# Kernel optimization log

Hardware: AMD Instinct MI355X
Metric: run time of the kernel (lower is better)

Reference implementation:

```python
import jax, jax.numpy as jnp
import numpy as np
import math

SR = 16000
FFT = 1024
WIN = 640
HOP = 320
NMEL = 40
NCEP = 13
B = 1024
NS = 16000
F_MIN = 0.0
F_MAX = 8000.0
LIFT_L = 22.0
DELTA_N = 2


def _linear_to_mel_weight_matrix(num_mel, num_spec_bins, sr, fmin, fmax):
    # Exact replica of tf.signal.linear_to_mel_weight_matrix (HTK mel scale).
    def hz_to_mel(f):
        return 1127.0 * np.log1p(np.asarray(f, np.float64) / 700.0)
    nyquist = sr / 2.0
    lin_freqs = np.linspace(0.0, nyquist, num_spec_bins)
    spec_mel = hz_to_mel(lin_freqs[1:])[:, None]          # drop DC bin
    edges = np.linspace(hz_to_mel(fmin), hz_to_mel(fmax), num_mel + 2)
    lower, center, upper = edges[:-2], edges[1:-1], edges[2:]
    lower_slope = (spec_mel - lower) / (center - lower)
    upper_slope = (upper - spec_mel) / (upper - center)
    w = np.maximum(0.0, np.minimum(lower_slope, upper_slope))
    w = np.pad(w, ((1, 0), (0, 0)))                       # re-add zero DC row
    return w.astype(np.float32)


def setup_inputs() -> dict:
    key = jax.random.key(0)
    waveforms = jax.random.normal(key, (B, NS), dtype=jnp.float32)
    mel_fb = jnp.asarray(_linear_to_mel_weight_matrix(NMEL, FFT // 2 + 1, SR, F_MIN, F_MAX))
    return {"waveforms": waveforms, "mel_fb": mel_fb}


def _delta(feat, N):
    # feat: (B, T, C). Replicate-pad N frames at both ends, then weighted
    # sliding-window sum with weights k in [-N..N] (vectorized, no map_fn).
    T = feat.shape[1]
    denom = 2.0 * sum(float(k * k) for k in range(1, N + 1))
    padded = jnp.concatenate(
        [jnp.repeat(feat[:, :1, :], N, axis=1), feat,
         jnp.repeat(feat[:, -1:, :], N, axis=1)], axis=1)
    acc = jnp.zeros_like(feat)
    for k in range(-N, N + 1):
        if k != 0:
            acc = acc + float(k) * padded[:, N + k:N + k + T, :]
    return acc / denom


def reference(waveforms, mel_fb):
    # --- STFT (tf.signal.stft: periodic Hann, no pad_end, zero-pad to FFT) ---
    n = jnp.arange(WIN, dtype=jnp.float32)
    window = 0.5 - 0.5 * jnp.cos(2.0 * math.pi * n / WIN)
    num_frames = 1 + (NS - WIN) // HOP                    # 49
    idx = jnp.arange(num_frames)[:, None] * HOP + jnp.arange(WIN)[None, :]
    frames = waveforms[:, idx] * window
    frames = jnp.pad(frames, ((0, 0), (0, 0), (0, FFT - WIN)))
    spec = jnp.abs(jnp.fft.rfft(frames, n=FFT, axis=-1))  # (B, T, 513)

    # --- mel + log ---
    log_mel = jnp.log(spec @ mel_fb + 1e-6)               # (B, T, NMEL)

    # --- MFCC: DCT-II scaled by rsqrt(2*NMEL), keep first NCEP coeffs ---
    m = jnp.arange(NMEL, dtype=jnp.float32)[:, None]
    k = jnp.arange(NCEP, dtype=jnp.float32)[None, :]
    dct_mat = 2.0 * jnp.cos(math.pi * (2.0 * m + 1.0) * k / (2.0 * NMEL))
    mfccs = (log_mel @ dct_mat) * (1.0 / math.sqrt(2.0 * NMEL))

    # --- liftering ---
    c = jnp.arange(NCEP, dtype=jnp.float32)
    lift = 1.0 + (LIFT_L / 2.0) * jnp.sin(math.pi * c / LIFT_L)
    mfccs = mfccs * lift

    # --- deltas and delta-deltas ---
    d1 = _delta(mfccs, DELTA_N)
    d2 = _delta(d1, DELTA_N)
    out = jnp.concatenate([mfccs, d1, d2], axis=2)        # (B, T, 3*NCEP)
    return out[..., None]                                 # (B, T, 39, 1)
```

## Files before the change

### kernel.cpp

```cpp
#include <hip/hip_runtime.h>
#include <math.h>

#define NMEL   40
#define NCEP   13
#define BATCH  1024
#define NSAMP  16000
#define NFRAME 49
#define PI_F   3.14159265358979323846f

#define WS_WIN  0
#define WS_R    640
#define WS_DT   1664
#define WS_BT   2184
#define WS_TOT  15240

typedef _Float16 half8 __attribute__((ext_vector_type(8)));
typedef __fp16   fp16x2 __attribute__((ext_vector_type(2)));
typedef float f32x4 __attribute__((ext_vector_type(4)));

#define WAVE_FENCE() { __builtin_amdgcn_wave_barrier(); asm volatile("" ::: "memory"); }

#define BFLY(i0, i1, wr, wi) {                        \
    float tr = zr[i0] - zr[i1], ti = zi[i0] - zi[i1]; \
    zr[i0] += zr[i1]; zi[i0] += zi[i1];               \
    zr[i1] = tr*(wr) - ti*(wi);                       \
    zi[i1] = tr*(wi) + ti*(wr); }

__device__ __forceinline__ unsigned pk_f16(float a, float b) {
    fp16x2 h = __builtin_amdgcn_cvt_pkrtz(a, b);
    union { fp16x2 h; unsigned u; } cvt; cvt.h = h;
    return cvt.u;
}

__global__ __launch_bounds__(256) void mfcc_prep(
    const float* __restrict__ mel_fb, float* __restrict__ ws)
{
    const int idx = blockIdx.x * 256 + threadIdx.x;

    _Float16* bt = (_Float16*)(ws + WS_BT);
    for (int i = idx; i < 48 * 544; i += 64 * 256) {
        int n = i / 544, k = i - n * 544;
        float v = (n < NMEL && k < 513) ? mel_fb[k * NMEL + n] : 0.0f;
        bt[i] = (_Float16)v;
    }

    if (idx < 640 + 512 + 520) {
        int i = idx;
        if (i < 640) {
            ws[WS_WIN + i] = 0.5f - 0.5f * cosf(2.0f * PI_F * (float)i / 640.0f);
        } else if (i < 1152) {
            int k = i - 640;
            float s, c;
            sincosf(-2.0f * PI_F * (float)k / 1024.0f, &s, &c);
            ((float2*)(ws + WS_R))[k] = make_float2(c, s);
        } else {
            int j = i - 1152;
            int m = j / 13, c0 = j - m * 13;
            float d    = 2.0f * cosf(PI_F * (2.0f * m + 1.0f) * (float)c0 / 80.0f);
            float lift = 1.0f + 11.0f * sinf(PI_F * (float)c0 / 22.0f);
            ws[WS_DT + j] = d * 0.11180339887498949f * lift;
        }
    }
}

__global__ __launch_bounds__(256) void mfcc_stage1(
    const float* __restrict__ wave, const float* __restrict__ ws,
    float* __restrict__ out)
{
    __shared__ __align__(16) char smem[4 * 640 * 8 + 16 * 40 * 2];
    char* smemc = smem;
    _Float16* lm = (_Float16*)(smem + 4 * 640 * 8);

    const int tid = threadIdx.x;
    const int wv  = tid >> 6;
    const int L   = tid & 63;
    const int s   = L & 7;
    const int a   = L >> 3;

    float2* Z = (float2*)smem + wv * 640;
    const float2* R   = (const float2*)(ws + WS_R);
    const float2* win = (const float2*)(ws + WS_WIN);

    float2 twA[4], twB[2], twC, twD[4], twE[2], twF, twS[8], winv[5];
    #pragma unroll
    for (int j = 0; j < 4; ++j) twA[j] = R[2 * (L + 64 * j)];
    #pragma unroll
    for (int j = 0; j < 2; ++j) twB[j] = R[4 * (L + 64 * j)];
    twC = R[8 * L];
    #pragma unroll
    for (int j = 0; j < 4; ++j) twD[j] = R[128 * j + 16 * s];
    #pragma unroll
    for (int j = 0; j < 2; ++j) twE[j] = R[256 * j + 32 * s];
    twF = R[64 * s];
    #pragma unroll
    for (int j = 0; j < 8; ++j) twS[j] = R[8 * L + j];
    #pragma unroll
    for (int j = 0; j < 5; ++j) winv[j] = win[L + 64 * j];

    uint4 mgp[4];
    float m512v[4] = {0.0f, 0.0f, 0.0f, 0.0f};

    #pragma unroll
    for (int fi = 0; fi < 4; ++fi) {
        const int frame = blockIdx.x * 16 + wv * 4 + fi;
        const int b = frame / NFRAME;
        const int f = frame - b * NFRAME;
        const float2* xin = (const float2*)(wave + (size_t)b * NSAMP + (size_t)f * 320);

        float zr[8], zi[8];
        #pragma unroll
        for (int j = 0; j < 8; ++j) { zr[j] = 0.0f; zi[j] = 0.0f; }
        #pragma unroll
        for (int j = 0; j < 5; ++j) {
            float2 x = xin[L + 64 * j];
            zr[j] = x.x * winv[j].x;
            zi[j] = x.y * winv[j].y;
        }

        #pragma unroll
        for (int j = 0; j < 4; ++j) BFLY(j, j + 4, twA[j].x, twA[j].y);
        #pragma unroll
        for (int g = 0; g < 8; g += 4) {
            #pragma unroll
            for (int j = 0; j < 2; ++j) BFLY(g + j, g + j + 2, twB[j].x, twB[j].y);
        }
        #pragma unroll
        for (int i0 = 0; i0 < 8; i0 += 2) BFLY(i0, i0 + 1, twC.x, twC.y);

        WAVE_FENCE();
        #pragma unroll
        for (int j = 0; j < 8; ++j)
            Z[80 * j + 10 * s + a] = make_float2(zr[j], zi[j]);
        WAVE_FENCE();
        {
            float4 q0 = *(float4*)&Z[10 * L + 0];
            float4 q1 = *(float4*)&Z[10 * L + 2];
            float4 q2 = *(float4*)&Z[10 * L + 4];
            float4 q3 = *(float4*)&Z[10 * L + 6];
            zr[0] = q0.x; zi[0] = q0.y; zr[1] = q0.z; zi[1] = q0.w;
            zr[2] = q1.x; zi[2] = q1.y; zr[3] = q1.z; zi[3] = q1.w;
            zr[4] = q2.x; zi[4] = q2.y; zr[5] = q2.z; zi[5] = q2.w;
            zr[6] = q3.x; zi[6] = q3.y; zr[7] = q3.z; zi[7] = q3.w;
        }

        #pragma unroll
        for (int j = 0; j < 4; ++j) BFLY(j, j + 4, twD[j].x, twD[j].y);
        #pragma unroll
        for (int g = 0; g < 8; g += 4) {
            #pragma unroll
            for (int j = 0; j < 2; ++j) BFLY(g + j, g + j + 2, twE[j].x, twE[j].y);
        }
        #pragma unroll
        for (int i0 = 0; i0 < 8; i0 += 2) BFLY(i0, i0 + 1, twF.x, twF.y);

        WAVE_FENCE();
        #pragma unroll
        for (int j = 0; j < 8; ++j)
            Z[80 * a + 10 * j + s] = make_float2(zr[j], zi[j]);
        WAVE_FENCE();
        {
            float4 q0 = *(float4*)&Z[10 * L + 0];
            float4 q1 = *(float4*)&Z[10 * L + 2];
            float4 q2 = *(float4*)&Z[10 * L + 4];
            float4 q3 = *(float4*)&Z[10 * L + 6];
            zr[0] = q0.x; zi[0] = q0.y; zr[1] = q0.z; zi[1] = q0.w;
            zr[2] = q1.x; zi[2] = q1.y; zr[3] = q1.z; zi[3] = q1.w;
            zr[4] = q2.x; zi[4] = q2.y; zr[5] = q2.z; zi[5] = q2.w;
            zr[6] = q3.x; zi[6] = q3.y; zr[7] = q3.z; zi[7] = q3.w;
        }

        {
            const float C = 0.70710678118654752f;
            const float w8r[4] = { 1.0f,  C, 0.0f, -C };
            const float w8i[4] = { 0.0f, -C, -1.0f, -C };
            #pragma unroll
            for (int j = 0; j < 4; ++j) BFLY(j, j + 4, w8r[j], w8i[j]);
            #pragma unroll
            for (int g = 0; g < 8; g += 4) {
                BFLY(g + 0, g + 2, 1.0f, 0.0f);
                BFLY(g + 1, g + 3, 0.0f, -1.0f);
            }
            #pragma unroll
            for (int i0 = 0; i0 < 8; i0 += 2) BFLY(i0, i0 + 1, 1.0f, 0.0f);
        }

        WAVE_FENCE();
        {
            const int rev3t[8] = { 0, 4, 2, 6, 1, 5, 3, 7 };
            int r6 = (int)(__brev((unsigned)L) >> 26);
            int u  = r6 + 2 * (r6 >> 3);
            #pragma unroll
            for (int j = 0; j < 8; ++j)
                Z[80 * rev3t[j] + u] = make_float2(zr[j], zi[j]);
        }
        WAVE_FENCE();

        float Ax[8], Ay[8], Bx[8], By[8];
        {
            float4 a0 = *(float4*)&Z[10 * L + 0];
            float4 a1 = *(float4*)&Z[10 * L + 2];
            float4 a2 = *(float4*)&Z[10 * L + 4];
            float4 a3 = *(float4*)&Z[10 * L + 6];
            Ax[0] = a0.x; Ay[0] = a0.y; Ax[1] = a0.z; Ay[1] = a0.w;
            Ax[2] = a1.x; Ay[2] = a1.y; Ax[3] = a1.z; Ay[3] = a1.w;
            Ax[4] = a2.x; Ay[4] = a2.y; Ax[5] = a2.z; Ay[5] = a2.w;
            Ax[6] = a3.x; Ay[6] = a3.y; Ax[7] = a3.z; Ay[7] = a3.w;
            float4 t0 = *(float4*)&Z[630 - 10 * L + 0];
            float4 t1 = *(float4*)&Z[630 - 10 * L + 2];
            float4 t2 = *(float4*)&Z[630 - 10 * L + 4];
            float4 t3 = *(float4*)&Z[630 - 10 * L + 6];
            float2 b0 = Z[640 - 10 * L];
            Bx[0] = b0.x;  By[0] = b0.y;
            Bx[7] = t0.z;  By[7] = t0.w;
            Bx[6] = t1.x;  By[6] = t1.y;
            Bx[5] = t1.z;  By[5] = t1.w;
            Bx[4] = t2.x;  By[4] = t2.y;
            Bx[3] = t2.z;  By[3] = t2.w;
            Bx[2] = t3.x;  By[2] = t3.y;
            Bx[1] = t3.z;  By[1] = t3.w;
        }
        float mg[8];
        #pragma unroll
        for (int j = 0; j < 8; ++j) {
            int k = 8 * L + j;
            if (k == 0) {
                mg[j]     = fabsf(Ax[0] + Ay[0]);
                m512v[fi] = fabsf(Ax[0] - Ay[0]);
            } else {
                float xer = 0.5f * (Ax[j] + Bx[j]), xei = 0.5f * (Ay[j] - By[j]);
                float xo  = 0.5f * (Ay[j] + By[j]), xoi = -0.5f * (Ax[j] - Bx[j]);
                float xr = xer + twS[j].x * xo - twS[j].y * xoi;
                float xi = xei + twS[j].x * xoi + twS[j].y * xo;
                mg[j] = sqrtf(xr * xr + xi * xi);
            }
        }
        mgp[fi].x = pk_f16(mg[0], mg[1]);
        mgp[fi].y = pk_f16(mg[2], mg[3]);
        mgp[fi].z = pk_f16(mg[4], mg[5]);
        mgp[fi].w = pk_f16(mg[6], mg[7]);
        WAVE_FENCE();
    }

    __syncthreads();
    #pragma unroll
    for (int fi = 0; fi < 4; ++fi) {
        const int row = wv * 4 + fi;
        *(uint4*)(smemc + row * 1104 + 16 * L) = mgp[fi];
        if (L < 20) {
            unsigned v = (L == 0) ? pk_f16(m512v[fi], 0.0f) : 0u;
            *(unsigned*)(smemc + row * 1104 + 1024 + 4 * L) = v;
        }
    }
    __syncthreads();

    if (wv < 3) {
        const int nl = L & 15, q = L >> 4;
        const char* ap = smemc + nl * 1104 + q * 16;
        const _Float16* btp = (const _Float16*)(ws + WS_BT)
                              + (size_t)(wv * 16 + nl) * 544 + q * 8;
        f32x4 acc = {0.0f, 0.0f, 0.0f, 0.0f};
        #pragma unroll
        for (int kk = 0; kk < 17; ++kk) {
            half8 av = *(const half8*)(ap + kk * 64);
            half8 bv = *(const half8*)(btp + kk * 32);
            acc = __builtin_amdgcn_mfma_f32_16x16x32_f16(av, bv, acc, 0, 0, 0);
        }
        const int mel = wv * 16 + nl;
        if (mel < NMEL) {
            #pragma unroll
            for (int r = 0; r < 4; ++r) {
                int fl = q * 4 + r;
                lm[fl * NMEL + mel] = (_Float16)__logf(acc[r] + 1e-6f);
            }
        }
    }
    __syncthreads();

    if (tid < 16 * NCEP) {
        const int fl = tid / NCEP, c = tid - fl * NCEP;
        float acc = 0.0f;
        #pragma unroll
        for (int m = 0; m < NMEL; ++m)
            acc += (float)lm[fl * NMEL + m] * ws[WS_DT + m * 13 + c];
        out[(size_t)(blockIdx.x * 16 + fl) * (3 * NCEP) + c] = acc;
    }
}

__global__ __launch_bounds__(128) void mfcc_stage2(float* __restrict__ out)
{
    __shared__ float x [NFRAME * NCEP];
    __shared__ float d1[NFRAME * NCEP];

    const int b = blockIdx.x;
    const int tid = threadIdx.x;
    const int TC = NFRAME * NCEP;

    for (int i = tid; i < TC; i += 128) {
        const int t = i / NCEP, c = i - t * NCEP;
        x[i] = out[((size_t)b * NFRAME + t) * (3 * NCEP) + c];
    }
    __syncthreads();

    for (int i = tid; i < TC; i += 128) {
        const int t = i / NCEP, c = i - t * NCEP;
        float acc = 0.0f;
        #pragma unroll
        for (int k = -2; k <= 2; ++k) {
            if (k == 0) continue;
            int tt = t + k;
            tt = tt < 0 ? 0 : (tt > NFRAME - 1 ? NFRAME - 1 : tt);
            acc += (float)k * x[tt * NCEP + c];
        }
        d1[i] = acc * 0.1f;
    }
    __syncthreads();

    for (int i = tid; i < TC; i += 128) {
        const int t = i / NCEP, c = i - t * NCEP;
        float acc = 0.0f;
        #pragma unroll
        for (int k = -2; k <= 2; ++k) {
            if (k == 0) continue;
            int tt = t + k;
            tt = tt < 0 ? 0 : (tt > NFRAME - 1 ? NFRAME - 1 : tt);
            acc += (float)k * d1[tt * NCEP + c];
        }
        const size_t base = ((size_t)b * NFRAME + t) * (3 * NCEP);
        out[base +     NCEP + c] = d1[i];
        out[base + 2 * NCEP + c] = acc * 0.1f;
    }
}

extern "C" void kernel_launch(void* const* d_in, const int* in_sizes, int n_in,
                              void* d_out, int out_size, void* d_ws, size_t ws_size,
                              hipStream_t stream)
{
    const float* wave   = (const float*)d_in[0];
    const float* mel_fb = (const float*)d_in[1];
    float* out = (float*)d_out;
    float* ws  = (float*)d_ws;

    mfcc_prep<<<64, 256, 0, stream>>>(mel_fb, ws);
    mfcc_stage1<<<(BATCH * NFRAME) / 16, 256, 0, stream>>>(wave, ws, out);
    mfcc_stage2<<<BATCH, 128, 0, stream>>>(out);
}
```

Baseline: 176.4 us.

## Fuse STFT/mel/DCT stage with delta computation into one per-batch kernel

Merges the two stages into a single kernel with one block per batch item. The block loops over four chunks of 16 frames, doing FFT, mel MFMA and DCT, and keeps the cepstra in shared memory so the deltas can be computed without a global round trip or a second launch. The cost is wasted work: the last chunk holds only one valid frame, so three of its four waves idle. The grid also drops from 3136 blocks to 1024, with more serial work per block and more shared memory per block.

```diff
diff --git a/kernel.cpp b/kernel.cpp
--- a/kernel.cpp
+++ b/kernel.cpp
@@ -63,19 +63,22 @@
     }
 }
 
-__global__ __launch_bounds__(256) void mfcc_stage1(
+__global__ __launch_bounds__(256) void mfcc_fused(
     const float* __restrict__ wave, const float* __restrict__ ws,
     float* __restrict__ out)
 {
-    __shared__ __align__(16) char smem[4 * 640 * 8 + 16 * 40 * 2];
+    __shared__ __align__(16) char smem[4 * 640 * 8];
+    __shared__ _Float16 lm[NFRAME * NMEL];
+    __shared__ float cep[NFRAME * NCEP];
+    __shared__ float d1b[NFRAME * NCEP];
+
     char* smemc = smem;
-    _Float16* lm = (_Float16*)(smem + 4 * 640 * 8);
-
     const int tid = threadIdx.x;
     const int wv  = tid >> 6;
     const int L   = tid & 63;
     const int s   = L & 7;
     const int a   = L >> 3;
+    const int b   = blockIdx.x;
 
     float2* Z = (float2*)smem + wv * 640;
     const float2* R   = (const float2*)(ws + WS_R);
@@ -97,237 +100,234 @@
     #pragma unroll
     for (int j = 0; j < 5; ++j) winv[j] = win[L + 64 * j];
 
-    uint4 mgp[4];
-    float m512v[4] = {0.0f, 0.0f, 0.0f, 0.0f};
-
-    #pragma unroll
-    for (int fi = 0; fi < 4; ++fi) {
-        const int frame = blockIdx.x * 16 + wv * 4 + fi;
-        const int b = frame / NFRAME;
-        const int f = frame - b * NFRAME;
-        const float2* xin = (const float2*)(wave + (size_t)b * NSAMP + (size_t)f * 320);
-
-        float zr[8], zi[8];
-        #pragma unroll
-        for (int j = 0; j < 8; ++j) { zr[j] = 0.0f; zi[j] = 0.0f; }
-        #pragma unroll
-        for (int j = 0; j < 5; ++j) {
-            float2 x = xin[L + 64 * j];
-            zr[j] = x.x * winv[j].x;
-            zi[j] = x.y * winv[j].y;
-        }
-
-        #pragma unroll
-        for (int j = 0; j < 4; ++j) BFLY(j, j + 4, twA[j].x, twA[j].y);
-        #pragma unroll
-        for (int g = 0; g < 8; g += 4) {
+    for (int c = 0; c < 4; ++c) {
+        const int f0 = c * 16 + wv * 4;
+        uint4 mgp[4];
+        float m512v[4] = {0.0f, 0.0f, 0.0f, 0.0f};
+
+        if (f0 < NFRAME) {
             #pragma unroll
-            for (int j = 0; j < 2; ++j) BFLY(g + j, g + j + 2, twB[j].x, twB[j].y);
-        }
-        #pragma unroll
-        for (int i0 = 0; i0 < 8; i0 += 2) BFLY(i0, i0 + 1, twC.x, twC.y);
-
-        WAVE_FENCE();
-        #pragma unroll
-        for (int j = 0; j < 8; ++j)
-            Z[80 * j + 10 * s + a] = make_float2(zr[j], zi[j]);
-        WAVE_FENCE();
-        {
-            float4 q0 = *(float4*)&Z[10 * L + 0];
-            float4 q1 = *(float4*)&Z[10 * L + 2];
-            float4 q2 = *(float4*)&Z[10 * L + 4];
-            float4 q3 = *(float4*)&Z[10 * L + 6];
-            zr[0] = q0.x; zi[0] = q0.y; zr[1] = q0.z; zi[1] = q0.w;
-            zr[2] = q1.x; zi[2] = q1.y; zr[3] = q1.z; zi[3] = q1.w;
-            zr[4] = q2.x; zi[4] = q2.y; zr[5] = q2.z; zi[5] = q2.w;
-            zr[6] = q3.x; zi[6] = q3.y; zr[7] = q3.z; zi[7] = q3.w;
-        }
-
-        #pragma unroll
-        for (int j = 0; j < 4; ++j) BFLY(j, j + 4, twD[j].x, twD[j].y);
-        #pragma unroll
-        for (int g = 0; g < 8; g += 4) {
+            for (int fi = 0; fi < 4; ++fi) {
+                const int f = f0 + fi;
+                if (f >= NFRAME) continue;
+                const float2* xin = (const float2*)(wave + (size_t)b * NSAMP + (size_t)f * 320);
+
+                float zr[8], zi[8];
+                #pragma unroll
+                for (int j = 0; j < 8; ++j) { zr[j] = 0.0f; zi[j] = 0.0f; }
+                #pragma unroll
+                for (int j = 0; j < 5; ++j) {
+                    float2 x = xin[L + 64 * j];
+                    zr[j] = x.x * winv[j].x;
+                    zi[j] = x.y * winv[j].y;
+                }
+
+                #pragma unroll
+                for (int j = 0; j < 4; ++j) BFLY(j, j + 4, twA[j].x, twA[j].y);
+                #pragma unroll
+                for (int g = 0; g < 8; g += 4) {
+                    #pragma unroll
+                    for (int j = 0; j < 2; ++j) BFLY(g + j, g + j + 2, twB[j].x, twB[j].y);
+                }
+                #pragma unroll
+                for (int i0 = 0; i0 < 8; i0 += 2) BFLY(i0, i0 + 1, twC.x, twC.y);
+
+                WAVE_FENCE();
+                #pragma unroll
+                for (int j = 0; j < 8; ++j)
+                    Z[80 * j + 10 * s + a] = make_float2(zr[j], zi[j]);
+                WAVE_FENCE();
+                {
+                    float4 q0 = *(float4*)&Z[10 * L + 0];
+                    float4 q1 = *(float4*)&Z[10 * L + 2];
+                    float4 q2 = *(float4*)&Z[10 * L + 4];
+                    float4 q3 = *(float4*)&Z[10 * L + 6];
+                    zr[0] = q0.x; zi[0] = q0.y; zr[1] = q0.z; zi[1] = q0.w;
+                    zr[2] = q1.x; zi[2] = q1.y; zr[3] = q1.z; zi[3] = q1.w;
+                    zr[4] = q2.x; zi[4] = q2.y; zr[5] = q2.z; zi[5] = q2.w;
+                    zr[6] = q3.x; zi[6] = q3.y; zr[7] = q3.z; zi[7] = q3.w;
+                }
+
+                #pragma unroll
+                for (int j = 0; j < 4; ++j) BFLY(j, j + 4, twD[j].x, twD[j].y);
+                #pragma unroll
+                for (int g = 0; g < 8; g += 4) {
+                    #pragma unroll
+                    for (int j = 0; j < 2; ++j) BFLY(g + j, g + j + 2, twE[j].x, twE[j].y);
+                }
+                #pragma unroll
+                for (int i0 = 0; i0 < 8; i0 += 2) BFLY(i0, i0 + 1, twF.x, twF.y);
+
+                WAVE_FENCE();
+                #pragma unroll
+                for (int j = 0; j < 8; ++j)
+                    Z[80 * a + 10 * j + s] = make_float2(zr[j], zi[j]);
+                WAVE_FENCE();
+                {
+                    float4 q0 = *(float4*)&Z[10 * L + 0];
+                    float4 q1 = *(float4*)&Z[10 * L + 2];
+                    float4 q2 = *(float4*)&Z[10 * L + 4];
+                    float4 q3 = *(float4*)&Z[10 * L + 6];
+                    zr[0] = q0.x; zi[0] = q0.y; zr[1] = q0.z; zi[1] = q0.w;
+                    zr[2] = q1.x; zi[2] = q1.y; zr[3] = q1.z; zi[3] = q1.w;
+                    zr[4] = q2.x; zi[4] = q2.y; zr[5] = q2.z; zi[5] = q2.w;
+                    zr[6] = q3.x; zi[6] = q3.y; zr[7] = q3.z; zi[7] = q3.w;
+                }
+
+                {
+                    const float C = 0.70710678118654752f;
+                    const float w8r[4] = { 1.0f,  C, 0.0f, -C };
+                    const float w8i[4] = { 0.0f, -C, -1.0f, -C };
+                    #pragma unroll
+                    for (int j = 0; j < 4; ++j) BFLY(j, j + 4, w8r[j], w8i[j]);
+                    #pragma unroll
+                    for (int g = 0; g < 8; g += 4) {
+                        BFLY(g + 0, g + 2, 1.0f, 0.0f);
+                        BFLY(g + 1, g + 3, 0.0f, -1.0f);
+                    }
+                    #pragma unroll
+                    for (int i0 = 0; i0 < 8; i0 += 2) BFLY(i0, i0 + 1, 1.0f, 0.0f);
+                }
+
+                WAVE_FENCE();
+                {
+                    const int rev3t[8] = { 0, 4, 2, 6, 1, 5, 3, 7 };
+                    int r6 = (int)(__brev((unsigned)L) >> 26);
+                    int u  = r6 + 2 * (r6 >> 3);
+                    #pragma unroll
+                    for (int j = 0; j < 8; ++j)
+                        Z[80 * rev3t[j] + u] = make_float2(zr[j], zi[j]);
+                }
+                WAVE_FENCE();
+
+                float Ax[8], Ay[8], Bx[8], By[8];
+                {
+                    float4 a0 = *(float4*)&Z[10 * L + 0];
+                    float4 a1 = *(float4*)&Z[10 * L + 2];
+                    float4 a2 = *(float4*)&Z[10 * L + 4];
+                    float4 a3 = *(float4*)&Z[10 * L + 6];
+                    Ax[0] = a0.x; Ay[0] = a0.y; Ax[1] = a0.z; Ay[1] = a0.w;
+                    Ax[2] = a1.x; Ay[2] = a1.y; Ax[3] = a1.z; Ay[3] = a1.w;
+                    Ax[4] = a2.x; Ay[4] = a2.y; Ax[5] = a2.z; Ay[5] = a2.w;
+                    Ax[6] = a3.x; Ay[6] = a3.y; Ax[7] = a3.z; Ay[7] = a3.w;
+                    float4 t0 = *(float4*)&Z[630 - 10 * L + 0];
+                    float4 t1 = *(float4*)&Z[630 - 10 * L + 2];
+                    float4 t2 = *(float4*)&Z[630 - 10 * L + 4];
+                    float4 t3 = *(float4*)&Z[630 - 10 * L + 6];
+                    float2 b0 = Z[640 - 10 * L];
+                    Bx[0] = b0.x;  By[0] = b0.y;
+                    Bx[7] = t0.z;  By[7] = t0.w;
+                    Bx[6] = t1.x;  By[6] = t1.y;
+                    Bx[5] = t1.z;  By[5] = t1.w;
+                    Bx[4] = t2.x;  By[4] = t2.y;
+                    Bx[3] = t2.z;  By[3] = t2.w;
+                    Bx[2] = t3.x;  By[2] = t3.y;
+                    Bx[1] = t3.z;  By[1] = t3.w;
+                }
+                float mg[8];
+                #pragma unroll
+                for (int j = 0; j < 8; ++j) {
+                    int k = 8 * L + j;
+                    if (k == 0) {
+                        mg[j]     = fabsf(Ax[0] + Ay[0]);
+                        m512v[fi] = fabsf(Ax[0] - Ay[0]);
+                    } else {
+                        float xer = 0.5f * (Ax[j] + Bx[j]), xei = 0.5f * (Ay[j] - By[j]);
+                        float xo  = 0.5f * (Ay[j] + By[j]), xoi = -0.5f * (Ax[j] - Bx[j]);
+                        float xr = xer + twS[j].x * xo - twS[j].y * xoi;
+                        float xi = xei + twS[j].x * xoi + twS[j].y * xo;
+                        mg[j] = sqrtf(xr * xr + xi * xi);
+                    }
+                }
+                mgp[fi].x = pk_f16(mg[0], mg[1]);
+                mgp[fi].y = pk_f16(mg[2], mg[3]);
+                mgp[fi].z = pk_f16(mg[4], mg[5]);
+                mgp[fi].w = pk_f16(mg[6], mg[7]);
+                WAVE_FENCE();
+            }
+        }
+
+        __syncthreads();
+        if (f0 < NFRAME) {
             #pragma unroll
-            for (int j = 0; j < 2; ++j) BFLY(g + j, g + j + 2, twE[j].x, twE[j].y);
-        }
-        #pragma unroll
-        for (int i0 = 0; i0 < 8; i0 += 2) BFLY(i0, i0 + 1, twF.x, twF.y);
-
-        WAVE_FENCE();
-        #pragma unroll
-        for (int j = 0; j < 8; ++j)
-            Z[80 * a + 10 * j + s] = make_float2(zr[j], zi[j]);
-        WAVE_FENCE();
-        {
-            float4 q0 = *(float4*)&Z[10 * L + 0];
-            float4 q1 = *(float4*)&Z[10 * L + 2];
-            float4 q2 = *(float4*)&Z[10 * L + 4];
-            float4 q3 = *(float4*)&Z[10 * L + 6];
-            zr[0] = q0.x; zi[0] = q0.y; zr[1] = q0.z; zi[1] = q0.w;
-            zr[2] = q1.x; zi[2] = q1.y; zr[3] = q1.z; zi[3] = q1.w;
-            zr[4] = q2.x; zi[4] = q2.y; zr[5] = q2.z; zi[5] = q2.w;
-            zr[6] = q3.x; zi[6] = q3.y; zr[7] = q3.z; zi[7] = q3.w;
-        }
-
-        {
-            const float C = 0.70710678118654752f;
-            const float w8r[4] = { 1.0f,  C, 0.0f, -C };
-            const float w8i[4] = { 0.0f, -C, -1.0f, -C };
+            for (int fi = 0; fi < 4; ++fi) {
+                if (f0 + fi >= NFRAME) continue;
+                const int row = wv * 4 + fi;
+                *(uint4*)(smemc + row * 1104 + 16 * L) = mgp[fi];
+                if (L < 20) {
+                    unsigned v = (L == 0) ? pk_f16(m512v[fi], 0.0f) : 0u;
+                    *(unsigned*)(smemc + row * 1104 + 1024 + 4 * L) = v;
+                }
+            }
+        }
+        __syncthreads();
+
+        if (wv < 3) {
+            const int nl = L & 15, q = L >> 4;
+            const char* ap = smemc + nl * 1104 + q * 16;
+            const _Float16* btp = (const _Float16*)(ws + WS_BT)
+                                  + (size_t)(wv * 16 + nl) * 544 + q * 8;
+            f32x4 acc = {0.0f, 0.0f, 0.0f, 0.0f};
             #pragma unroll
-            for (int j = 0; j < 4; ++j) BFLY(j, j + 4, w8r[j], w8i[j]);
-            #pragma unroll
-            for (int g = 0; g < 8; g += 4) {
-                BFLY(g + 0, g + 2, 1.0f, 0.0f);
-                BFLY(g + 1, g + 3, 0.0f, -1.0f);
-            }
-            #pragma unroll
-            for (int i0 = 0; i0 < 8; i0 += 2) BFLY(i0, i0 + 1, 1.0f, 0.0f);
-        }
-
-        WAVE_FENCE();
-        {
-            const int rev3t[8] = { 0, 4, 2, 6, 1, 5, 3, 7 };
-            int r6 = (int)(__brev((unsigned)L) >> 26);
-            int u  = r6 + 2 * (r6 >> 3);
-            #pragma unroll
-            for (int j = 0; j < 8; ++j)
-                Z[80 * rev3t[j] + u] = make_float2(zr[j], zi[j]);
-        }
-        WAVE_FENCE();
-
-        float Ax[8], Ay[8], Bx[8], By[8];
-        {
-            float4 a0 = *(float4*)&Z[10 * L + 0];
-            float4 a1 = *(float4*)&Z[10 * L + 2];
-            float4 a2 = *(float4*)&Z[10 * L + 4];
-            float4 a3 = *(float4*)&Z[10 * L + 6];
-            Ax[0] = a0.x; Ay[0] = a0.y; Ax[1] = a0.z; Ay[1] = a0.w;
-            Ax[2] = a1.x; Ay[2] = a1.y; Ax[3] = a1.z; Ay[3] = a1.w;
-            Ax[4] = a2.x; Ay[4] = a2.y; Ax[5] = a2.z; Ay[5] = a2.w;
-            Ax[6] = a3.x; Ay[6] = a3.y; Ax[7] = a3.z; Ay[7] = a3.w;
-            float4 t0 = *(float4*)&Z[630 - 10 * L + 0];
-            float4 t1 = *(float4*)&Z[630 - 10 * L + 2];
-            float4 t2 = *(float4*)&Z[630 - 10 * L + 4];
-            float4 t3 = *(float4*)&Z[630 - 10 * L + 6];
-            float2 b0 = Z[640 - 10 * L];
-            Bx[0] = b0.x;  By[0] = b0.y;
-            Bx[7] = t0.z;  By[7] = t0.w;
-            Bx[6] = t1.x;  By[6] = t1.y;
-            Bx[5] = t1.z;  By[5] = t1.w;
-            Bx[4] = t2.x;  By[4] = t2.y;
-            Bx[3] = t2.z;  By[3] = t2.w;
-            Bx[2] = t3.x;  By[2] = t3.y;
-            Bx[1] = t3.z;  By[1] = t3.w;
-        }
-        float mg[8];
-        #pragma unroll
-        for (int j = 0; j < 8; ++j) {
-            int k = 8 * L + j;
-            if (k == 0) {
-                mg[j]     = fabsf(Ax[0] + Ay[0]);
-                m512v[fi] = fabsf(Ax[0] - Ay[0]);
-            } else {
-                float xer = 0.5f * (Ax[j] + Bx[j]), xei = 0.5f * (Ay[j] - By[j]);
-                float xo  = 0.5f * (Ay[j] + By[j]), xoi = -0.5f * (Ax[j] - Bx[j]);
-                float xr = xer + twS[j].x * xo - twS[j].y * xoi;
-                float xi = xei + twS[j].x * xoi + twS[j].y * xo;
-                mg[j] = sqrtf(xr * xr + xi * xi);
-            }
-        }
-        mgp[fi].x = pk_f16(mg[0], mg[1]);
-        mgp[fi].y = pk_f16(mg[2], mg[3]);
-        mgp[fi].z = pk_f16(mg[4], mg[5]);
-        mgp[fi].w = pk_f16(mg[6], mg[7]);
-        WAVE_FENCE();
-    }
-
-    __syncthreads();
-    #pragma unroll
-    for (int fi = 0; fi < 4; ++fi) {
-        const int row = wv * 4 + fi;
-        *(uint4*)(smemc + row * 1104 + 16 * L) = mgp[fi];
-        if (L < 20) {
-            unsigned v = (L == 0) ? pk_f16(m512v[fi], 0.0f) : 0u;
-            *(unsigned*)(smemc + row * 1104 + 1024 + 4 * L) = v;
-        }
-    }
-    __syncthreads();
-
-    if (wv < 3) {
-        const int nl = L & 15, q = L >> 4;
-        const char* ap = smemc + nl * 1104 + q * 16;
-        const _Float16* btp = (const _Float16*)(ws + WS_BT)
-                              + (size_t)(wv * 16 + nl) * 544 + q * 8;
-        f32x4 acc = {0.0f, 0.0f, 0.0f, 0.0f};
-        #pragma unroll
-        for (int kk = 0; kk < 17; ++kk) {
-            half8 av = *(const half8*)(ap + kk * 64);
-            half8 bv = *(const half8*)(btp + kk * 32);
-            acc = __builtin_amdgcn_mfma_f32_16x16x32_f16(av, bv, acc, 0, 0, 0);
-        }
-        const int mel = wv * 16 + nl;
-        if (mel < NMEL) {
-            #pragma unroll
-            for (int r = 0; r < 4; ++r) {
-                int fl = q * 4 + r;
-                lm[fl * NMEL + mel] = (_Float16)__logf(acc[r] + 1e-6f);
-            }
-        }
-    }
-    __syncthreads();
-
-    if (tid < 16 * NCEP) {
-        const int fl = tid / NCEP, c = tid - fl * NCEP;
-        float acc = 0.0f;
-        #pragma unroll
-        for (int m = 0; m < NMEL; ++m)
-            acc += (float)lm[fl * NMEL + m] * ws[WS_DT + m * 13 + c];
-        out[(size_t)(blockIdx.x * 16 + fl) * (3 * NCEP) + c] = acc;
-    }
-}
-
-__global__ __launch_bounds__(128) void mfcc_stage2(float* __restrict__ out)
-{
-    __shared__ float x [NFRAME * NCEP];
-    __shared__ float d1[NFRAME * NCEP];
-
-    const int b = blockIdx.x;
-    const int tid = threadIdx.x;
+            for (int kk = 0; kk < 17; ++kk) {
+                half8 av = *(const half8*)(ap + kk * 64);
+                half8 bv = *(const half8*)(btp + kk * 32);
+                acc = __builtin_amdgcn_mfma_f32_16x16x32_f16(av, bv, acc, 0, 0, 0);
+            }
+            const int mel = wv * 16 + nl;
+            if (mel < NMEL) {
+                #pragma unroll
+                for (int r = 0; r < 4; ++r) {
+                    int frame = c * 16 + q * 4 + r;
+                    if (frame < NFRAME)
+                        lm[frame * NMEL + mel] = (_Float16)__logf(acc[r] + 1e-6f);
+                }
+            }
+        }
+        __syncthreads();
+
+        if (tid < 16 * NCEP) {
+            const int fl = tid / NCEP, cc = tid - fl * NCEP;
+            const int frame = c * 16 + fl;
+            if (frame < NFRAME) {
+                float acc = 0.0f;
+                #pragma unroll
+                for (int m = 0; m < NMEL; ++m)
+                    acc += (float)lm[frame * NMEL + m] * ws[WS_DT + m * 13 + cc];
+                cep[frame * NCEP + cc] = acc;
+            }
+        }
+        __syncthreads();
+    }
+
     const int TC = NFRAME * NCEP;
-
-    for (int i = tid; i < TC; i += 128) {
-        const int t = i / NCEP, c = i - t * NCEP;
-        x[i] = out[((size_t)b * NFRAME + t) * (3 * NCEP) + c];
-    }
-    __syncthreads();
-
-    for (int i = tid; i < TC; i += 128) {
-        const int t = i / NCEP, c = i - t * NCEP;
+    for (int i = tid; i < TC; i += 256) {
+        const int t = i / NCEP, cc = i - t * NCEP;
         float acc = 0.0f;
         #pragma unroll
         for (int k = -2; k <= 2; ++k) {
             if (k == 0) continue;
             int tt = t + k;
             tt = tt < 0 ? 0 : (tt > NFRAME - 1 ? NFRAME - 1 : tt);
-            acc += (float)k * x[tt * NCEP + c];
-        }
-        d1[i] = acc * 0.1f;
+            acc += (float)k * cep[tt * NCEP + cc];
+        }
+        d1b[i] = acc * 0.1f;
     }
     __syncthreads();
-
-    for (int i = tid; i < TC; i += 128) {
-        const int t = i / NCEP, c = i - t * NCEP;
+    for (int i = tid; i < TC; i += 256) {
+        const int t = i / NCEP, cc = i - t * NCEP;
         float acc = 0.0f;
         #pragma unroll
         for (int k = -2; k <= 2; ++k) {
             if (k == 0) continue;
             int tt = t + k;
             tt = tt < 0 ? 0 : (tt > NFRAME - 1 ? NFRAME - 1 : tt);
-            acc += (float)k * d1[tt * NCEP + c];
+            acc += (float)k * d1b[tt * NCEP + cc];
         }
         const size_t base = ((size_t)b * NFRAME + t) * (3 * NCEP);
-        out[base +     NCEP + c] = d1[i];
-        out[base + 2 * NCEP + c] = acc * 0.1f;
+        out[base +            cc] = cep[i];
+        out[base +     NCEP + cc] = d1b[i];
+        out[base + 2 * NCEP + cc] = acc * 0.1f;
     }
 }
 
@@ -341,6 +341,5 @@
     float* ws  = (float*)d_ws;
 
     mfcc_prep<<<64, 256, 0, stream>>>(mel_fb, ws);
-    mfcc_stage1<<<(BATCH * NFRAME) / 16, 256, 0, stream>>>(wave, ws, out);
-    mfcc_stage2<<<BATCH, 128, 0, stream>>>(out);
+    mfcc_fused<<<BATCH, 256, 0, stream>>>(wave, ws, out);
 }
```

New measurement: 253.3 us. +43.6%, slower.
